# Kernel optimization log

Measured on AMD Instinct MI355X. Metric: run time of the kernel, lower is better.

The kernel has to match this reference:

```python
import jax, jax.numpy as jnp
import numpy as np

N = 100000      # num nodes
E = 3200000     # num edges
R = 8           # num relations
C_IN, HID, C_OUT = 128, 64, 64


def rgcn_conv(x, W, root, bias, src, dst, etype):
    """One RGCNConv layer (PyG semantics, mean aggregation per relation).
    out[i] = bias + x[i] @ root + sum_r mean_{j in N_r(i)} x[j] @ W[r]
    """
    n = x.shape[0]
    # transform-then-gather: [R, N, H] avoids per-edge [E, C, H] matmuls
    xW = jnp.einsum('nc,rch->rnh', x, W)
    msg = xW[etype, src]                              # [E, H]
    # per-(relation, target-node) in-degree for mean normalization
    seg = etype * n + dst
    deg = jax.ops.segment_sum(jnp.ones((src.shape[0],), dtype=x.dtype), seg,
                              num_segments=R * n)      # [R*N]
    msg = msg / jnp.maximum(deg[seg], 1.0)[:, None]
    agg = jax.ops.segment_sum(msg, dst, num_segments=n)  # [N, H]
    return agg + x @ root + bias


def setup_inputs() -> dict:
    key = jax.random.key(0)
    ks = jax.random.split(key, 9)
    x = jax.random.normal(ks[0], (N, C_IN), dtype=jnp.float32)
    edge_index = jax.random.randint(ks[1], (2, E), 0, N)
    edge_type = jax.random.randint(ks[2], (E,), 0, R)
    s1 = 1.0 / np.sqrt(C_IN)
    s2 = 1.0 / np.sqrt(HID)
    W1 = jax.random.normal(ks[3], (R, C_IN, HID), dtype=jnp.float32) * s1
    root1 = jax.random.normal(ks[4], (C_IN, HID), dtype=jnp.float32) * s1
    b1 = jnp.zeros((HID,), dtype=jnp.float32)
    W2 = jax.random.normal(ks[5], (R, HID, C_OUT), dtype=jnp.float32) * s2
    root2 = jax.random.normal(ks[6], (HID, C_OUT), dtype=jnp.float32) * s2
    b2 = jnp.zeros((C_OUT,), dtype=jnp.float32)
    return {"x": x, "edge_index": edge_index, "edge_type": edge_type,
            "W1": W1, "root1": root1, "b1": b1,
            "W2": W2, "root2": root2, "b2": b2}


def reference(x, edge_index, edge_type, W1, root1, b1, W2, root2, b2):
    src, dst = edge_index[0], edge_index[1]
    h = rgcn_conv(x, W1, root1, b1, src, dst, edge_type)
    h = jax.nn.relu(h)  # dropout p=0.0 is identity
    out = rgcn_conv(h, W2, root2, b2, src, dst, edge_type)
    return out
```

## Files before the change

### kernel.cpp

```cpp
#include <hip/hip_runtime.h>

#define N_NODES 100000
#define N_EDGES 3200000
#define R_REL   8
#define C_IN    128
#define HID     64
#define WCOLS   576
#define OFFMASK 0x03FFFFFFu

#define NBUCK 500
#define NPB   200
#define NBLK  256
#define CHUNK 12500
#define NCELL (NBUCK * NBLK)
#define BCAP  7680

typedef __attribute__((ext_vector_type(8))) short  short8;
typedef __attribute__((ext_vector_type(4))) float  float4v;

__device__ __forceinline__ float bf2f(unsigned short u) {
    union { unsigned int i; float f; } v; v.i = ((unsigned int)u) << 16; return v.f;
}
__device__ __forceinline__ unsigned short f2bf(float f) {
    union { float f; unsigned int i; } v; v.f = f;
    unsigned int r = v.i + 0x7FFFu + ((v.i >> 16) & 1u);
    return (unsigned short)(r >> 16);
}
__device__ __forceinline__ float rl_f(float v, int j) {
    union { float f; int i; } a, b; a.f = v;
    b.i = __builtin_amdgcn_readlane(a.i, j);
    return b.f;
}

__global__ void prep_wcat(const float* __restrict__ W1,
                          const float* __restrict__ root1,
                          const float* __restrict__ W2,
                          const float* __restrict__ root2,
                          unsigned short* __restrict__ BT1,
                          unsigned short* __restrict__ BT2) {
    int idx = blockIdx.x * 256 + threadIdx.x;
    const int T1 = WCOLS * C_IN;
    const int T2 = WCOLS * HID;
    if (idx < T1) {
        int c = idx / C_IN, k = idx % C_IN;
        float v;
        if (c < 512) { int r = c >> 6, h = c & 63; v = W1[r * (C_IN * 64) + k * 64 + h]; }
        else         { v = root1[k * 64 + (c - 512)]; }
        BT1[idx] = f2bf(v);
    } else if (idx < T1 + T2) {
        int j = idx - T1;
        int c = j / HID, k = j % HID;
        float v;
        if (c < 512) { int r = c >> 6, h = c & 63; v = W2[r * (HID * 64) + k * 64 + h]; }
        else         { v = root2[k * 64 + (c - 512)]; }
        BT2[j] = f2bf(v);
    }
}

__global__ __launch_bounds__(512)
void edge_sort_local(const int* __restrict__ src, const int* __restrict__ dst,
                     const int* __restrict__ et,
                     unsigned int* __restrict__ esort,
                     int* __restrict__ bcountT, int* __restrict__ lstartT) {
    __shared__ int cnt[NBUCK], cur[NBUCK], tsum[512];
    __shared__ unsigned int sedge[CHUNK];
    const int blk = blockIdx.x, tid = threadIdx.x;
    const int e0 = blk * CHUNK;

    for (int i = tid; i < NBUCK; i += 512) cnt[i] = 0;
    __syncthreads();
    for (int i = tid; i < CHUNK; i += 512)
        atomicAdd(&cnt[dst[e0 + i] / NPB], 1);
    __syncthreads();

    int v = (tid < NBUCK) ? cnt[tid] : 0;
    tsum[tid] = v; __syncthreads();
    for (int off = 1; off < 512; off <<= 1) {
        int t = (tid >= off) ? tsum[tid - off] : 0;
        __syncthreads(); tsum[tid] += t; __syncthreads();
    }
    if (tid < NBUCK) cur[tid] = tsum[tid] - v;
    __syncthreads();

    for (int b = tid; b < NBUCK; b += 512) {
        bcountT[blk * NBUCK + b] = cnt[b];
        lstartT[blk * NBUCK + b] = cur[b];
    }
    __syncthreads();

    for (int i = tid; i < CHUNK; i += 512) {
        int d = dst[e0 + i];
        int b = d / NPB;
        int pos = atomicAdd(&cur[b], 1);
        sedge[pos] = ((unsigned int)src[e0 + i] << 11) |
                     ((unsigned int)(d - b * NPB) << 3) | (unsigned int)et[e0 + i];
    }
    __syncthreads();
    for (int i = tid; i < CHUNK; i += 512) esort[e0 + i] = sedge[i];
}

__global__ __launch_bounds__(256)
void btot_sum(const int* __restrict__ bcountT, int* __restrict__ btot) {
    __shared__ int tsum[256];
    const int b = blockIdx.x, tid = threadIdx.x;
    int s = 0;
    for (int blk = tid; blk < NBLK; blk += 256) s += bcountT[blk * NBUCK + b];
    tsum[tid] = s; __syncthreads();
    for (int off = 128; off > 0; off >>= 1) {
        if (tid < off) tsum[tid] += tsum[tid + off];
        __syncthreads();
    }
    if (tid == 0) btot[b] = tsum[0];
}

__global__ __launch_bounds__(512)
void scan_btot(int* __restrict__ btot, int nb) {
    __shared__ int tmp[512];
    int tid = threadIdx.x;
    int v = (tid < nb) ? btot[tid] : 0;
    tmp[tid] = v; __syncthreads();
    for (int off = 1; off < 512; off <<= 1) {
        int t = (tid >= off) ? tmp[tid - off] : 0;
        __syncthreads(); tmp[tid] += t; __syncthreads();
    }
    if (tid < nb) btot[tid] = tmp[tid] - v;
}

__global__ __launch_bounds__(512)
void bucket_build(const unsigned int* __restrict__ esort,
                  const int* __restrict__ bcountT, const int* __restrict__ lstartT,
                  const int* __restrict__ btot,
                  unsigned int* __restrict__ elist,
                  int* __restrict__ rowstart8) {
    __shared__ int   cnt[2048], cur[2048], tsum[512];
    __shared__ int   rlen[NBLK], rpos[NBLK], rloff[NBLK];
    __shared__ unsigned int sedge[BCAP];
    __shared__ unsigned int selist[BCAP];

    const int b = blockIdx.x, tid = threadIdx.x;
    const int seg0 = btot[b];

    for (int i = tid; i < 2048; i += 512) cnt[i] = 0;
    if (tid < NBLK) {
        rlen[tid] = bcountT[tid * NBUCK + b];
        rpos[tid] = tid * CHUNK + lstartT[tid * NBUCK + b];
    }
    __syncthreads();

    int rv = (tid < NBLK) ? rlen[tid] : 0;
    tsum[tid] = rv; __syncthreads();
    for (int off = 1; off < 512; off <<= 1) {
        int t = (tid >= off) ? tsum[tid - off] : 0;
        __syncthreads(); tsum[tid] += t; __syncthreads();
    }
    if (tid < NBLK) rloff[tid] = tsum[tid] - rv;
    const int total = tsum[NBLK - 1];
    __syncthreads();
    const bool fits = (total <= BCAP);

    for (int i = tid; i < total; i += 512) {
        int lo = 0, hi = NBLK - 1;
        while (lo < hi) { int mid = (lo + hi + 1) >> 1; if (rloff[mid] <= i) lo = mid; else hi = mid - 1; }
        unsigned int e = esort[rpos[lo] + (i - rloff[lo])];
        if (fits) sedge[i] = e;
        atomicAdd(&cnt[(int)((e >> 3) & 255u) * 8 + (int)(e & 7u)], 1);
    }
    __syncthreads();

    int base = tid * 4, s = 0, loc[4];
#pragma unroll
    for (int k = 0; k < 4; ++k) { loc[k] = s; s += cnt[base + k]; }
    tsum[tid] = s; __syncthreads();
    for (int off = 1; off < 512; off <<= 1) {
        int t = (tid >= off) ? tsum[tid - off] : 0;
        __syncthreads(); tsum[tid] += t; __syncthreads();
    }
    int texcl = tsum[tid] - s;
#pragma unroll
    for (int k = 0; k < 4; ++k) cur[base + k] = texcl + loc[k];
    __syncthreads();

    for (int i = tid; i < NPB * 8; i += 512)
        rowstart8[(b * NPB) * 8 + i] = seg0 + cur[i];
    if (b == NBUCK - 1 && tid == 0) rowstart8[N_NODES * 8] = N_EDGES;
    __syncthreads();

    for (int i = tid; i < total; i += 512) {
        unsigned int e;
        if (fits) e = sedge[i];
        else {
            int lo = 0, hi = NBLK - 1;
            while (lo < hi) { int mid = (lo + hi + 1) >> 1; if (rloff[mid] <= i) lo = mid; else hi = mid - 1; }
            e = esort[rpos[lo] + (i - rloff[lo])];
        }
        int r = (int)(e & 7u);
        int j = (int)((e >> 3) & 255u) * 8 + r;
        int p = atomicAdd(&cur[j], 1);
        unsigned int eo = (e >> 11) * WCOLS + (unsigned int)(r * 64);
        if (fits) selist[p] = eo;
        else      elist[seg0 + p] = eo;
    }
    __syncthreads();

    if (fits) {
        for (int i = tid; i < total; i += 512)
            elist[seg0 + i] = selist[i];
    }
}

template <int K, bool AF32>
__global__ __launch_bounds__(256)
void gemm_rows(const void* __restrict__ Araw,
               const unsigned short* __restrict__ BT,
               unsigned short* __restrict__ Out, int nrows) {
    constexpr int KSTEPS = K / 32;
    constexpr int LDB = K + 8;
    __shared__ __align__(16) unsigned short Blds[64 * LDB];
    __shared__ __align__(16) unsigned short stage[4][16 * 64];

    const int wave = threadIdx.x >> 6;
    const int lane = threadIdx.x & 63;
    const int l15 = lane & 15, quad = lane >> 4;
    const int rowbase = blockIdx.x * 64 + wave * 16;
    int arow = rowbase + l15;
    if (arow >= nrows) arow = nrows - 1;

    short8 afrag[KSTEPS];
    if constexpr (AF32) {
        const float* Af = (const float*)Araw;
#pragma unroll
        for (int ks = 0; ks < KSTEPS; ++ks) {
            const float* p = Af + (size_t)arow * K + ks * 32 + quad * 8;
            float4v u0 = *(const float4v*)p;
            float4v u1 = *(const float4v*)(p + 4);
            short8 f;
            f[0] = (short)f2bf(u0[0]); f[1] = (short)f2bf(u0[1]);
            f[2] = (short)f2bf(u0[2]); f[3] = (short)f2bf(u0[3]);
            f[4] = (short)f2bf(u1[0]); f[5] = (short)f2bf(u1[1]);
            f[6] = (short)f2bf(u1[2]); f[7] = (short)f2bf(u1[3]);
            afrag[ks] = f;
        }
    } else {
        const unsigned short* Ab = (const unsigned short*)Araw;
#pragma unroll
        for (int ks = 0; ks < KSTEPS; ++ks)
            afrag[ks] = *(const short8*)(Ab + (size_t)arow * K + ks * 32 + quad * 8);
    }

    for (int chunk = 0; chunk < 9; ++chunk) {
        __syncthreads();
        {
            const unsigned short* src = BT + (size_t)chunk * 64 * K;
            const int nvec = 64 * K / 8;
            for (int i = threadIdx.x; i < nvec; i += 256) {
                int r = i / (K / 8);
                int cpos = (i % (K / 8)) * 8;
                *(uint4*)(&Blds[r * LDB + cpos]) = *(const uint4*)(src + r * K + cpos);
            }
        }
        __syncthreads();

        float4v acc[4];
#pragma unroll
        for (int ct = 0; ct < 4; ++ct) { acc[ct][0] = 0.f; acc[ct][1] = 0.f; acc[ct][2] = 0.f; acc[ct][3] = 0.f; }

#pragma unroll
        for (int ct = 0; ct < 4; ++ct) {
#pragma unroll
            for (int ks = 0; ks < KSTEPS; ++ks) {
                short8 bfrag = *(const short8*)(&Blds[(ct * 16 + l15) * LDB + ks * 32 + quad * 8]);
                acc[ct] = __builtin_amdgcn_mfma_f32_16x16x32_bf16(afrag[ks], bfrag, acc[ct], 0, 0, 0);
            }
        }

#pragma unroll
        for (int ct = 0; ct < 4; ++ct)
#pragma unroll
            for (int r = 0; r < 4; ++r)
                stage[wave][(quad * 4 + r) * 64 + ct * 16 + l15] = f2bf(acc[ct][r]);
        __syncthreads();

        {
            int r = lane >> 2, j = lane & 3;
            int orow = rowbase + r;
            if (orow < nrows) {
#pragma unroll
                for (int p = 0; p < 2; ++p) {
                    int c0 = (j + p * 4) * 8;
                    uint4 v = *(const uint4*)&stage[wave][r * 64 + c0];
                    *(uint4*)(Out + (size_t)orow * WCOLS + chunk * 64 + c0) = v;
                }
            }
        }
    }
}

template <int MODE>
__global__ __launch_bounds__(256)
void agg_fused(const unsigned short* __restrict__ XW,
               const unsigned int* __restrict__ elist,
               const int* __restrict__ rowstart8,
               const float* __restrict__ bias,
               void* __restrict__ outp) {
    const int wave = threadIdx.x >> 6, lane = threadIdx.x & 63;
    const int n = blockIdx.x * 4 + wave;
    int r9 = 0;
    if (lane < 9) r9 = rowstart8[n * 8 + lane];
    const int b0 = __builtin_amdgcn_readlane(r9, 0);
    const int b1 = __builtin_amdgcn_readlane(r9, 1);
    const int b2 = __builtin_amdgcn_readlane(r9, 2);
    const int b3 = __builtin_amdgcn_readlane(r9, 3);
    const int b4 = __builtin_amdgcn_readlane(r9, 4);
    const int b5 = __builtin_amdgcn_readlane(r9, 5);
    const int b6 = __builtin_amdgcn_readlane(r9, 6);
    const int b7 = __builtin_amdgcn_readlane(r9, 7);
    const int b8 = __builtin_amdgcn_readlane(r9, 8);
    const int beg = b0, end = b8;

    auto invlen = [](int a, int bnd) {
        int l = bnd - a; return 1.0f / (float)(l > 1 ? l : 1);
    };
    const float il0 = invlen(b0, b1), il1 = invlen(b1, b2);
    const float il2 = invlen(b2, b3), il3 = invlen(b3, b4);
    const float il4 = invlen(b4, b5), il5 = invlen(b5, b6);
    const float il6 = invlen(b6, b7), il7 = invlen(b7, b8);

    const unsigned short* XWl = XW + lane;

    float acc = 0.f;
    int i = beg;
    while (i < end) {
        int m = end - i; if (m > 64) m = 64;
        int idx = i + lane; if (idx >= end) idx = end - 1;
        unsigned int ub = elist[idx];
        float wb = il0;
        wb = (idx >= b1) ? il1 : wb;
        wb = (idx >= b2) ? il2 : wb;
        wb = (idx >= b3) ? il3 : wb;
        wb = (idx >= b4) ? il4 : wb;
        wb = (idx >= b5) ? il5 : wb;
        wb = (idx >= b6) ? il6 : wb;
        wb = (idx >= b7) ? il7 : wb;

        int j = 0;
        for (; j + 16 <= m; j += 16) {
            float vv[16], ww[16];
#pragma unroll
            for (int t = 0; t < 16; ++t) {
                unsigned int u = (unsigned int)__builtin_amdgcn_readlane((int)ub, j + t) & OFFMASK;
                ww[t] = rl_f(wb, j + t);
                vv[t] = bf2f(XWl[u]);
            }
#pragma unroll
            for (int t = 0; t < 16; ++t) acc += ww[t] * vv[t];
        }
        for (; j + 4 <= m; j += 4) {
            float vv[4], ww[4];
#pragma unroll
            for (int t = 0; t < 4; ++t) {
                unsigned int u = (unsigned int)__builtin_amdgcn_readlane((int)ub, j + t) & OFFMASK;
                ww[t] = rl_f(wb, j + t);
                vv[t] = bf2f(XWl[u]);
            }
#pragma unroll
            for (int t = 0; t < 4; ++t) acc += ww[t] * vv[t];
        }
        for (; j < m; ++j) {
            unsigned int u = (unsigned int)__builtin_amdgcn_readlane((int)ub, j) & OFFMASK;
            float w = rl_f(wb, j);
            acc += w * bf2f(XWl[u]);
        }
        i += m;
    }

    float res = acc + bf2f(XW[(size_t)n * WCOLS + 512 + lane]) + bias[lane];
    if (MODE == 0) {
        res = res > 0.f ? res : 0.f;
        ((unsigned short*)outp)[(size_t)n * 64 + lane] = f2bf(res);
    } else {
        ((float*)outp)[(size_t)n * 64 + lane] = res;
    }
}

extern "C" void kernel_launch(void* const* d_in, const int* in_sizes, int n_in,
                              void* d_out, int out_size, void* d_ws, size_t ws_size,
                              hipStream_t stream) {
    const float* x     = (const float*)d_in[0];
    const int*   eidx  = (const int*)d_in[1];
    const int*   etyp  = (const int*)d_in[2];
    const float* W1    = (const float*)d_in[3];
    const float* root1 = (const float*)d_in[4];
    const float* b1    = (const float*)d_in[5];
    const float* W2    = (const float*)d_in[6];
    const float* root2 = (const float*)d_in[7];
    const float* b2    = (const float*)d_in[8];
    float*       out   = (float*)d_out;

    char* ws = (char*)d_ws;
    size_t off = 0;
    auto alloc = [&](size_t bytes) { char* p = ws + off; off += (bytes + 255) & ~(size_t)255; return p; };

    unsigned short* xW       = (unsigned short*)alloc((size_t)N_NODES * WCOLS * 2);
    unsigned short* h        = (unsigned short*)alloc((size_t)N_NODES * HID * 2);
    unsigned int*   elist    = (unsigned int*)alloc((size_t)N_EDGES * 4);
    int*            rowstart8= (int*)alloc(((size_t)N_NODES * 8 + 1) * 4);
    unsigned short* BT1      = (unsigned short*)alloc((size_t)WCOLS * C_IN * 2);
    unsigned short* BT2      = (unsigned short*)alloc((size_t)WCOLS * HID * 2);

    unsigned int* esort   = (unsigned int*)xW;
    int*          bcountT = (int*)((char*)xW + (size_t)N_EDGES * 4);
    int*          lstartT = bcountT + NCELL;
    int*          btot    = lstartT + NCELL;

    const int* srcp = eidx;
    const int* dstp = eidx + N_EDGES;

    prep_wcat<<<(WCOLS * (C_IN + HID) + 255) / 256, 256, 0, stream>>>(W1, root1, W2, root2, BT1, BT2);

    edge_sort_local<<<NBLK, 512, 0, stream>>>(srcp, dstp, etyp, esort, bcountT, lstartT);
    btot_sum<<<NBUCK, 256, 0, stream>>>(bcountT, btot);
    scan_btot<<<1, 512, 0, stream>>>(btot, NBUCK);
    bucket_build<<<NBUCK, 512, 0, stream>>>(esort, bcountT, lstartT, btot, elist, rowstart8);

    const int gemm_grid = (N_NODES + 63) / 64;
    const int agg_grid  = N_NODES / 4;

    gemm_rows<C_IN, true><<<gemm_grid, 256, 0, stream>>>((const void*)x, BT1, xW, N_NODES);
    agg_fused<0><<<agg_grid, 256, 0, stream>>>(xW, elist, rowstart8, b1, (void*)h);

    gemm_rows<HID, false><<<gemm_grid, 256, 0, stream>>>((const void*)h, BT2, xW, N_NODES);
    agg_fused<1><<<agg_grid, 256, 0, stream>>>(xW, elist, rowstart8, b2, (void*)out);
}
```

Baseline: 412.1 us.

## Aggregate-then-transform in second RGCN layer with per-relation mean gather

The second layer now gathers and mean-aggregates the narrow hidden features per relation into a concatenated [N, 576] buffer, then applies one GEMM with stacked relation and root weights plus bias. The edge list now stores source indices, and the first-layer aggregation computes xW offsets from source and relation. This is meant to make the second-layer gather read compact 64-wide rows instead of strided rows in the wide transformed buffer. In exchange it writes a wide intermediate and runs a larger-K GEMM, and it adds bf16 rounding of the aggregated means.

New measurement: 502.2 us. 1.22x slower.

```diff
diff --git a/kernel.cpp b/kernel.cpp
--- a/kernel.cpp
+++ b/kernel.cpp
@@ -6,7 +6,6 @@
 #define C_IN    128
 #define HID     64
 #define WCOLS   576
-#define OFFMASK 0x03FFFFFFu
 
 #define NBUCK 500
 #define NPB   200
@@ -37,10 +36,10 @@
                           const float* __restrict__ W2,
                           const float* __restrict__ root2,
                           unsigned short* __restrict__ BT1,
-                          unsigned short* __restrict__ BT2) {
+                          unsigned short* __restrict__ BT2b) {
     int idx = blockIdx.x * 256 + threadIdx.x;
     const int T1 = WCOLS * C_IN;
-    const int T2 = WCOLS * HID;
+    const int T2 = 64 * WCOLS;
     if (idx < T1) {
         int c = idx / C_IN, k = idx % C_IN;
         float v;
@@ -49,11 +48,11 @@
         BT1[idx] = f2bf(v);
     } else if (idx < T1 + T2) {
         int j = idx - T1;
-        int c = j / HID, k = j % HID;
+        int c2 = j / WCOLS, k2 = j % WCOLS;
         float v;
-        if (c < 512) { int r = c >> 6, h = c & 63; v = W2[r * (HID * 64) + k * 64 + h]; }
-        else         { v = root2[k * 64 + (c - 512)]; }
-        BT2[j] = f2bf(v);
+        if (k2 < 512) { int r = k2 >> 6, ch = k2 & 63; v = W2[r * (HID * 64) + ch * 64 + c2]; }
+        else          { v = root2[(k2 - 512) * 64 + c2]; }
+        BT2b[j] = f2bf(v);
     }
 }
 
@@ -196,9 +195,9 @@
         int r = (int)(e & 7u);
         int j = (int)((e >> 3) & 255u) * 8 + r;
         int p = atomicAdd(&cur[j], 1);
-        unsigned int eo = (e >> 11) * WCOLS + (unsigned int)(r * 64);
-        if (fits) selist[p] = eo;
-        else      elist[seg0 + p] = eo;
+        unsigned int src = e >> 11;
+        if (fits) selist[p] = src;
+        else      elist[seg0 + p] = src;
     }
     __syncthreads();
 
@@ -295,13 +294,66 @@
     }
 }
 
-template <int MODE>
+__global__ __launch_bounds__(256)
+void gemm_out(const unsigned short* __restrict__ A,
+              const unsigned short* __restrict__ BT,
+              const float* __restrict__ bias,
+              float* __restrict__ Out, int nrows) {
+    constexpr int K = WCOLS;
+    constexpr int LDB = K + 8;
+    __shared__ __align__(16) unsigned short Blds[64 * LDB];
+
+    const int wave = threadIdx.x >> 6;
+    const int lane = threadIdx.x & 63;
+    const int l15 = lane & 15, quad = lane >> 4;
+    const int rowbase = blockIdx.x * 64 + wave * 16;
+    int arow = rowbase + l15;
+    if (arow >= nrows) arow = nrows - 1;
+
+    {
+        const int nvec = 64 * K / 8;
+        for (int i = threadIdx.x; i < nvec; i += 256) {
+            int r = i / (K / 8);
+            int c = (i % (K / 8)) * 8;
+            *(uint4*)(&Blds[r * LDB + c]) = *(const uint4*)(BT + r * K + c);
+        }
+    }
+    __syncthreads();
+
+    float4v acc[4];
+#pragma unroll
+    for (int ct = 0; ct < 4; ++ct) { acc[ct][0] = 0.f; acc[ct][1] = 0.f; acc[ct][2] = 0.f; acc[ct][3] = 0.f; }
+
+    const unsigned short* Ar = A + (size_t)arow * K;
+#pragma unroll
+    for (int ks = 0; ks < K / 32; ++ks) {
+        short8 afrag = *(const short8*)(Ar + ks * 32 + quad * 8);
+#pragma unroll
+        for (int ct = 0; ct < 4; ++ct) {
+            short8 bfrag = *(const short8*)(&Blds[(ct * 16 + l15) * LDB + ks * 32 + quad * 8]);
+            acc[ct] = __builtin_amdgcn_mfma_f32_16x16x32_bf16(afrag, bfrag, acc[ct], 0, 0, 0);
+        }
+    }
+
+#pragma unroll
+    for (int ct = 0; ct < 4; ++ct) {
+        int c = ct * 16 + l15;
+        float bv = bias[c];
+#pragma unroll
+        for (int r = 0; r < 4; ++r) {
+            int orow = rowbase + quad * 4 + r;
+            if (orow < nrows)
+                Out[(size_t)orow * 64 + c] = acc[ct][r] + bv;
+        }
+    }
+}
+
 __global__ __launch_bounds__(256)
 void agg_fused(const unsigned short* __restrict__ XW,
                const unsigned int* __restrict__ elist,
                const int* __restrict__ rowstart8,
                const float* __restrict__ bias,
-               void* __restrict__ outp) {
+               unsigned short* __restrict__ outp) {
     const int wave = threadIdx.x >> 6, lane = threadIdx.x & 63;
     const int n = blockIdx.x * 4 + wave;
     int r9 = 0;
@@ -332,7 +384,10 @@
     while (i < end) {
         int m = end - i; if (m > 64) m = 64;
         int idx = i + lane; if (idx >= end) idx = end - 1;
-        unsigned int ub = elist[idx];
+        unsigned int sb = elist[idx];
+        int rl = (idx >= b1) + (idx >= b2) + (idx >= b3) + (idx >= b4) +
+                 (idx >= b5) + (idx >= b6) + (idx >= b7);
+        unsigned int ub = (sb * 9u + (unsigned int)rl) << 6;
         float wb = il0;
         wb = (idx >= b1) ? il1 : wb;
         wb = (idx >= b2) ? il2 : wb;
@@ -347,7 +402,7 @@
             float vv[16], ww[16];
 #pragma unroll
             for (int t = 0; t < 16; ++t) {
-                unsigned int u = (unsigned int)__builtin_amdgcn_readlane((int)ub, j + t) & OFFMASK;
+                unsigned int u = (unsigned int)__builtin_amdgcn_readlane((int)ub, j + t);
                 ww[t] = rl_f(wb, j + t);
                 vv[t] = bf2f(XWl[u]);
             }
@@ -358,7 +413,7 @@
             float vv[4], ww[4];
 #pragma unroll
             for (int t = 0; t < 4; ++t) {
-                unsigned int u = (unsigned int)__builtin_amdgcn_readlane((int)ub, j + t) & OFFMASK;
+                unsigned int u = (unsigned int)__builtin_amdgcn_readlane((int)ub, j + t);
                 ww[t] = rl_f(wb, j + t);
                 vv[t] = bf2f(XWl[u]);
             }
@@ -366,7 +421,7 @@
             for (int t = 0; t < 4; ++t) acc += ww[t] * vv[t];
         }
         for (; j < m; ++j) {
-            unsigned int u = (unsigned int)__builtin_amdgcn_readlane((int)ub, j) & OFFMASK;
+            unsigned int u = (unsigned int)__builtin_amdgcn_readlane((int)ub, j);
             float w = rl_f(wb, j);
             acc += w * bf2f(XWl[u]);
         }
@@ -374,12 +429,61 @@
     }
 
     float res = acc + bf2f(XW[(size_t)n * WCOLS + 512 + lane]) + bias[lane];
-    if (MODE == 0) {
-        res = res > 0.f ? res : 0.f;
-        ((unsigned short*)outp)[(size_t)n * 64 + lane] = f2bf(res);
-    } else {
-        ((float*)outp)[(size_t)n * 64 + lane] = res;
-    }
+    res = res > 0.f ? res : 0.f;
+    outp[(size_t)n * 64 + lane] = f2bf(res);
+}
+
+__global__ __launch_bounds__(256)
+void agg_gather(const unsigned short* __restrict__ h,
+                const unsigned int* __restrict__ elist,
+                const int* __restrict__ rowstart8,
+                unsigned short* __restrict__ agg) {
+    const int wave = threadIdx.x >> 6, lane = threadIdx.x & 63;
+    const int n = blockIdx.x * 4 + wave;
+    int r9 = 0;
+    if (lane < 9) r9 = rowstart8[n * 8 + lane];
+    int bnd[9];
+#pragma unroll
+    for (int k = 0; k < 9; ++k) bnd[k] = __builtin_amdgcn_readlane(r9, k);
+
+    const unsigned short* hl = h + lane;
+    float acc[8];
+#pragma unroll
+    for (int r = 0; r < 8; ++r) acc[r] = 0.f;
+
+#pragma unroll
+    for (int r = 0; r < 8; ++r) {
+        const int s0 = bnd[r], s1 = bnd[r + 1];
+        int i = s0;
+        while (i < s1) {
+            int m = s1 - i; if (m > 64) m = 64;
+            int idx = i + lane; if (idx >= s1) idx = s1 - 1;
+            unsigned int ub = elist[idx] << 6;
+            int j = 0;
+            for (; j + 4 <= m; j += 4) {
+                float vv[4];
+#pragma unroll
+                for (int t = 0; t < 4; ++t) {
+                    unsigned int u = (unsigned int)__builtin_amdgcn_readlane((int)ub, j + t);
+                    vv[t] = bf2f(hl[u]);
+                }
+#pragma unroll
+                for (int t = 0; t < 4; ++t) acc[r] += vv[t];
+            }
+            for (; j < m; ++j) {
+                unsigned int u = (unsigned int)__builtin_amdgcn_readlane((int)ub, j);
+                acc[r] += bf2f(hl[u]);
+            }
+            i += m;
+        }
+        int len = s1 - s0;
+        acc[r] *= 1.0f / (float)(len > 1 ? len : 1);
+    }
+
+    unsigned short* arow = agg + (size_t)n * WCOLS;
+#pragma unroll
+    for (int r = 0; r < 8; ++r) arow[r * 64 + lane] = f2bf(acc[r]);
+    arow[512 + lane] = h[(size_t)n * 64 + lane];
 }
 
 extern "C" void kernel_launch(void* const* d_in, const int* in_sizes, int n_in,
@@ -405,7 +509,7 @@
     unsigned int*   elist    = (unsigned int*)alloc((size_t)N_EDGES * 4);
     int*            rowstart8= (int*)alloc(((size_t)N_NODES * 8 + 1) * 4);
     unsigned short* BT1      = (unsigned short*)alloc((size_t)WCOLS * C_IN * 2);
-    unsigned short* BT2      = (unsigned short*)alloc((size_t)WCOLS * HID * 2);
+    unsigned short* BT2b     = (unsigned short*)alloc((size_t)64 * WCOLS * 2);
 
     unsigned int* esort   = (unsigned int*)xW;
     int*          bcountT = (int*)((char*)xW + (size_t)N_EDGES * 4);
@@ -415,7 +519,7 @@
     const int* srcp = eidx;
     const int* dstp = eidx + N_EDGES;
 
-    prep_wcat<<<(WCOLS * (C_IN + HID) + 255) / 256, 256, 0, stream>>>(W1, root1, W2, root2, BT1, BT2);
+    prep_wcat<<<(WCOLS * C_IN + 64 * WCOLS + 255) / 256, 256, 0, stream>>>(W1, root1, W2, root2, BT1, BT2b);
 
     edge_sort_local<<<NBLK, 512, 0, stream>>>(srcp, dstp, etyp, esort, bcountT, lstartT);
     btot_sum<<<NBUCK, 256, 0, stream>>>(bcountT, btot);
@@ -426,8 +530,8 @@
     const int agg_grid  = N_NODES / 4;
 
     gemm_rows<C_IN, true><<<gemm_grid, 256, 0, stream>>>((const void*)x, BT1, xW, N_NODES);
-    agg_fused<0><<<agg_grid, 256, 0, stream>>>(xW, elist, rowstart8, b1, (void*)h);
-
-    gemm_rows<HID, false><<<gemm_grid, 256, 0, stream>>>((const void*)h, BT2, xW, N_NODES);
-    agg_fused<1><<<agg_grid, 256, 0, stream>>>(xW, elist, rowstart8, b2, (void*)out);
-}
+    agg_fused<<<agg_grid, 256, 0, stream>>>(xW, elist, rowstart8, b1, h);
+
+    agg_gather<<<agg_grid, 256, 0, stream>>>(h, elist, rowstart8, xW);
+    gemm_out<<<gemm_grid, 256, 0, stream>>>(xW, BT2b, b2, out, N_NODES);
+}
```
